# Kernel optimization log

Measured on AMD Instinct MI355X. Metric: run time of the kernel, lower is better.

The kernel has to match this reference:

```python
import jax, jax.numpy as jnp
import numpy as np

B, R, C, E, H = 2, 16, 512, 1024, 16
D = E // H  # head_dim = 64


def setup_inputs() -> dict:
    key = jax.random.key(0)
    ks = jax.random.split(key, 9)
    s = 1.0 / np.sqrt(E)
    return {
        "x": jax.random.normal(ks[0], (B, R, C, E), dtype=jnp.float32),
        "wq": jax.random.uniform(ks[1], (E, E), jnp.float32, -s, s),
        "bq": jax.random.uniform(ks[2], (E,), jnp.float32, -s, s),
        "wk": jax.random.uniform(ks[3], (E, E), jnp.float32, -s, s),
        "bk": jax.random.uniform(ks[4], (E,), jnp.float32, -s, s),
        "wv": jax.random.uniform(ks[5], (E, E), jnp.float32, -s, s),
        "bv": jax.random.uniform(ks[6], (E,), jnp.float32, -s, s),
        "wo": jax.random.uniform(ks[7], (E, E), jnp.float32, -s, s),
        "bo": jax.random.uniform(ks[8], (E,), jnp.float32, -s, s),
    }


def reference(x, wq, bq, wk, bk, wv, bv, wo, bo):
    b, r, c, e = x.shape
    # projections: [b,r,c,e] -> [b,r,h,c,d]
    def split_heads(t):
        return t.reshape(b, r, c, H, D).transpose(0, 1, 3, 2, 4)
    q = split_heads(x @ wq + bq)
    k = split_heads(x @ wk + bk)
    v = split_heads(x @ wv + bv)
    scale = 1.0 / jnp.sqrt(jnp.asarray(D, x.dtype))
    logits = jnp.einsum('brhqd,brhkd->brhqk', q, k) * scale
    probs = jax.nn.softmax(logits, axis=-1)
    ctx = jnp.einsum('brhqk,brhkd->brhqd', probs, v)
    ctx = ctx.transpose(0, 1, 3, 2, 4).reshape(b, r, c, e)
    return ctx @ wo + bo
```

## Files before the change

kernel.cpp:

```cpp
#include <hip/hip_runtime.h>
#include <hip/hip_bf16.h>
#include <hip/hip_fp16.h>
#include <math.h>

typedef _Float16 half8 __attribute__((ext_vector_type(8)));
typedef __attribute__((ext_vector_type(4))) float floatx4;

constexpr int Bc = 2, Rc = 16, Cc = 512, Ec = 1024, Hc = 16, Dc = 64;
constexpr int Mtok = Bc * Rc * Cc;
#define QSCALE 0.180336880111120425f

__device__ inline void gl_lds16(const void* g, void* l) {
  __builtin_amdgcn_global_load_lds(
      (const __attribute__((address_space(1))) void*)g,
      (__attribute__((address_space(3))) void*)l, 16, 0, 0);
}
__device__ inline unsigned short f2h(float f) {
  __half h = __float2half_rn(f);
  return *(unsigned short*)&h;
}
__device__ inline unsigned int pack_h2(float lo, float hi) {
  __half2 p = __float22half2_rn(make_float2(lo, hi));
  return *(unsigned int*)&p;
}

__global__ __launch_bounds__(256) void cvt_x(const float* __restrict__ x,
                                             unsigned short* __restrict__ xh) {
  const size_t base = ((size_t)blockIdx.x * 256 + threadIdx.x) * 8;
  float4 a = *(const float4*)(x + base);
  float4 b = *(const float4*)(x + base + 4);
  uint4 o;
  o.x = pack_h2(a.x, a.y);
  o.y = pack_h2(a.z, a.w);
  o.z = pack_h2(b.x, b.y);
  o.w = pack_h2(b.z, b.w);
  *(uint4*)(xh + base) = o;
}

__global__ __launch_bounds__(256) void wprep(
    const float* __restrict__ w0, const float* __restrict__ w1,
    const float* __restrict__ w2, const float* __restrict__ w3,
    unsigned short* __restrict__ t0, unsigned short* __restrict__ t1,
    unsigned short* __restrict__ t2, unsigned short* __restrict__ t3) {
  __shared__ float tile[64][65];
  const int z = blockIdx.z;
  const float* W = (z == 0) ? w0 : (z == 1) ? w1 : (z == 2) ? w2 : w3;
  unsigned short* T = (z == 0) ? t0 : (z == 1) ? t1 : (z == 2) ? t2 : t3;
  const int tid = threadIdx.x;
  const int bk = blockIdx.x * 64, bn = blockIdx.y * 64;
#pragma unroll
  for (int p = 0; p < 16; ++p) {
    int idx = p * 256 + tid;
    int lk = idx >> 6, ln = idx & 63;
    tile[ln][lk] = W[(size_t)(bk + lk) * 1024 + bn + ln];
  }
  __syncthreads();
#pragma unroll
  for (int p = 0; p < 16; ++p) {
    int idx = p * 256 + tid;
    int ln = idx >> 6, lk = idx & 63;
    T[(size_t)(bn + ln) * 1024 + bk + lk] = f2h(tile[ln][lk]);
  }
}

__global__ __launch_bounds__(256, 2) void gemm_qkv(
    const unsigned short* __restrict__ xh, const unsigned short* __restrict__ wqh,
    const unsigned short* __restrict__ wkh, const unsigned short* __restrict__ wvh,
    const float* __restrict__ bq, const float* __restrict__ bk,
    const float* __restrict__ bv, unsigned short* __restrict__ qout,
    unsigned short* __restrict__ kout, unsigned short* __restrict__ vout) {
  __shared__ unsigned short As[128 * 32];
  __shared__ unsigned short Bs[256 * 32];
  const int z = blockIdx.z;
  const unsigned short* Bp = (z == 0) ? wqh : (z == 1) ? wkh : wvh;
  const float* bias = (z == 0) ? bq : (z == 1) ? bk : bv;
  const int tid = threadIdx.x;
  const int wv_ = tid >> 6, ln = tid & 63;
  const int bn = blockIdx.x * 256, bm = blockIdx.y * 128;
  floatx4 acc[4][8];
#pragma unroll
  for (int i = 0; i < 4; ++i)
#pragma unroll
    for (int j = 0; j < 8; ++j) acc[i][j] = (floatx4)(0.f);

  const int wm = (wv_ >> 1) * 64, wn = (wv_ & 1) * 128;
  const int lr = ln & 15, quad = ln >> 4;
  const int fsl = ((quad ^ ((lr >> 1) & 3)) << 3);
  const int coff = (((ln & 3) ^ ((ln >> 3) & 3)) << 3);

  for (int t = 0; t < 32; ++t) {
    const int kk = t << 5;
#pragma unroll
    for (int is = 0; is < 2; ++is) {
      const int r0 = is * 64 + wv_ * 16;
      const int row = r0 + (ln >> 2);
      gl_lds16(xh + (size_t)(bm + row) * 1024 + kk + coff, As + r0 * 32);
    }
#pragma unroll
    for (int p = 0; p < 4; ++p) {
      const int r0 = p * 64 + wv_ * 16;
      const int row = r0 + (ln >> 2);
      gl_lds16(Bp + (size_t)(bn + row) * 1024 + kk + coff, Bs + r0 * 32);
    }
    __syncthreads();
    half8 af[4], bfr[8];
#pragma unroll
    for (int i = 0; i < 4; ++i)
      af[i] = *(const half8*)&As[(wm + i * 16 + lr) * 32 + fsl];
#pragma unroll
    for (int j = 0; j < 8; ++j)
      bfr[j] = *(const half8*)&Bs[(wn + j * 16 + lr) * 32 + fsl];
#pragma unroll
    for (int i = 0; i < 4; ++i)
#pragma unroll
      for (int j = 0; j < 8; ++j)
        acc[i][j] = __builtin_amdgcn_mfma_f32_16x16x32_f16(af[i], bfr[j],
                                                           acc[i][j], 0, 0, 0);
    __syncthreads();
  }

  const int q4 = quad * 4;
  const bool odd = ln & 1;
#pragma unroll
  for (int i = 0; i < 4; ++i) {
#pragma unroll
    for (int j = 0; j < 8; ++j) {
      const int col = bn + wn + j * 16 + lr;
      float v[4];
#pragma unroll
      for (int r = 0; r < 4; ++r) v[r] = acc[i][j][r] + bias[col];
      const int m0 = bm + wm + i * 16 + q4;
      const int h = col >> 6, d = col & 63;
      const int br = m0 >> 9, c0 = m0 & 511;
      const size_t hb = ((size_t)br * 16 + h) * 32768;
      if (z == 2) {
        uint2 o;
        o.x = pack_h2(v[0], v[1]);
        o.y = pack_h2(v[2], v[3]);
        *(uint2*)(vout + hb + (size_t)d * 512 + c0) = o;
      } else {
        unsigned short* outp = (z == 0) ? qout : kout;
        if (z == 0) {
#pragma unroll
          for (int r = 0; r < 4; ++r) v[r] *= QSCALE;
        }
#pragma unroll
        for (int rp = 0; rp < 2; ++rp) {
          float a = v[2 * rp], b = v[2 * rp + 1];
          float ax = __shfl_xor(a, 1), bx = __shfl_xor(b, 1);
          unsigned int u = odd ? pack_h2(bx, b) : pack_h2(a, ax);
          const int c = c0 + 2 * rp + (odd ? 1 : 0);
          const int dd = d & ~1;
          *(unsigned int*)(outp + hb + (size_t)c * 64 + dd) = u;
        }
      }
    }
  }
}

__global__ __launch_bounds__(256, 2) void gemm_out(
    const unsigned short* __restrict__ Ah, const unsigned short* __restrict__ Bh,
    const float* __restrict__ bias, float* __restrict__ Out) {
  __shared__ unsigned short As[128 * 32];
  __shared__ unsigned short Bs[256 * 32];
  const int tid = threadIdx.x;
  const int wv_ = tid >> 6, ln = tid & 63;
  const int bn = blockIdx.x * 256, bm = blockIdx.y * 128;
  floatx4 acc[4][8];
#pragma unroll
  for (int i = 0; i < 4; ++i)
#pragma unroll
    for (int j = 0; j < 8; ++j) acc[i][j] = (floatx4)(0.f);

  const int wm = (wv_ >> 1) * 64, wn = (wv_ & 1) * 128;
  const int lr = ln & 15, quad = ln >> 4;
  const int fsl = ((quad ^ ((lr >> 1) & 3)) << 3);
  const int coff = (((ln & 3) ^ ((ln >> 3) & 3)) << 3);

  for (int t = 0; t < 32; ++t) {
    const int kk = t << 5;
#pragma unroll
    for (int is = 0; is < 2; ++is) {
      const int r0 = is * 64 + wv_ * 16;
      const int row = r0 + (ln >> 2);
      gl_lds16(Ah + (size_t)(bm + row) * 1024 + kk + coff, As + r0 * 32);
    }
#pragma unroll
    for (int p = 0; p < 4; ++p) {
      const int r0 = p * 64 + wv_ * 16;
      const int row = r0 + (ln >> 2);
      gl_lds16(Bh + (size_t)(bn + row) * 1024 + kk + coff, Bs + r0 * 32);
    }
    __syncthreads();
    half8 af[4], bfr[8];
#pragma unroll
    for (int i = 0; i < 4; ++i)
      af[i] = *(const half8*)&As[(wm + i * 16 + lr) * 32 + fsl];
#pragma unroll
    for (int j = 0; j < 8; ++j)
      bfr[j] = *(const half8*)&Bs[(wn + j * 16 + lr) * 32 + fsl];
#pragma unroll
    for (int i = 0; i < 4; ++i)
#pragma unroll
      for (int j = 0; j < 8; ++j)
        acc[i][j] = __builtin_amdgcn_mfma_f32_16x16x32_f16(af[i], bfr[j],
                                                           acc[i][j], 0, 0, 0);
    __syncthreads();
  }

  const int q4 = (ln >> 4) * 4;
#pragma unroll
  for (int i = 0; i < 4; ++i)
#pragma unroll
    for (int j = 0; j < 8; ++j)
#pragma unroll
      for (int r = 0; r < 4; ++r) {
        const int m = bm + wm + i * 16 + q4 + r;
        const int col = bn + wn + j * 16 + lr;
        Out[(size_t)m * 1024 + col] = acc[i][j][r] + bias[col];
      }
}

__global__ __launch_bounds__(256, 2) void attn_mfma(
    const unsigned short* __restrict__ Qh, const unsigned short* __restrict__ Kb,
    const unsigned short* __restrict__ Vt, unsigned short* __restrict__ Ctx) {
  __shared__ unsigned short Ks[128 * 64];
  __shared__ unsigned short Vs[64 * 128];
  __shared__ unsigned short Ps[128][136];

  const int t = threadIdx.x;
  const int w = t >> 6, ln = t & 63;
  const int lane15 = ln & 15, quad = ln >> 4;
  const bool odd = ln & 1;
  const int bh = blockIdx.x >> 2;
  const int qb = (blockIdx.x & 3) * 128;

  half8 qf[2][2];
  {
    const size_t qbase =
        ((size_t)bh * 512 + qb + w * 32 + lane15) * 64 + quad * 8;
#pragma unroll
    for (int i = 0; i < 2; ++i)
#pragma unroll
      for (int c = 0; c < 2; ++c)
        qf[i][c] = *(const half8*)(Qh + qbase + (size_t)i * 16 * 64 + c * 32);
  }

  floatx4 oacc[2][4];
#pragma unroll
  for (int i = 0; i < 2; ++i)
#pragma unroll
    for (int dj = 0; dj < 4; ++dj) oacc[i][dj] = (floatx4)(0.f);
  float lsum[2][4];
#pragma unroll
  for (int i = 0; i < 2; ++i)
#pragma unroll
    for (int r = 0; r < 4; ++r) lsum[i][r] = 0.f;

  const unsigned short* kgb = Kb + (size_t)bh * 32768;
  const unsigned short* vgb = Vt + (size_t)bh * 32768;

  for (int kt = 0; kt < 512; kt += 128) {
    __syncthreads();
    {
      const unsigned short* kq = kgb + (size_t)kt * 64;
#pragma unroll
      for (int p = 0; p < 4; ++p) {
        const int s = p * 256 + t;
        const int kr = s >> 3, kc16 = s & 7;
        gl_lds16(kq + kr * 64 + ((kc16 ^ (kr & 7)) << 3), (char*)Ks + s * 16);
        const int vr = s >> 4, vc16 = s & 15;
        gl_lds16(vgb + vr * 512 + kt + ((vc16 ^ (vr & 15)) << 3),
                 (char*)Vs + s * 16);
      }
    }
    __syncthreads();

    floatx4 sacc[2][8];
#pragma unroll
    for (int i = 0; i < 2; ++i)
#pragma unroll
      for (int j = 0; j < 8; ++j) sacc[i][j] = (floatx4)(0.f);
#pragma unroll
    for (int j = 0; j < 8; ++j) {
      const int krow = j * 16 + lane15;
      const unsigned short* kr = Ks + krow * 64;
      half8 kf0 = *(const half8*)(kr + ((quad ^ (krow & 7)) << 3));
      half8 kf1 = *(const half8*)(kr + (((4 + quad) ^ (krow & 7)) << 3));
#pragma unroll
      for (int i = 0; i < 2; ++i) {
        sacc[i][j] = __builtin_amdgcn_mfma_f32_16x16x32_f16(qf[i][0], kf0,
                                                            sacc[i][j], 0, 0, 0);
        sacc[i][j] = __builtin_amdgcn_mfma_f32_16x16x32_f16(qf[i][1], kf1,
                                                            sacc[i][j], 0, 0, 0);
      }
    }

#pragma unroll
    for (int i = 0; i < 2; ++i) {
#pragma unroll
      for (int rp = 0; rp < 2; ++rp) {
        const int rA = rp * 2, rB = rA + 1;
        const int row = w * 32 + i * 16 + quad * 4 + rA + (odd ? 1 : 0);
        unsigned short* prow = &Ps[row][lane15 & ~1];
#pragma unroll
        for (int j = 0; j < 8; ++j) {
          const float pA = exp2f(sacc[i][j][rA]);
          const float pB = exp2f(sacc[i][j][rB]);
          lsum[i][rA] += pA;
          lsum[i][rB] += pB;
          const float an = __shfl_xor(pA, 1);
          const float bn = __shfl_xor(pB, 1);
          const float lo = odd ? bn : pA;
          const float hi = odd ? pB : an;
          *(unsigned int*)(prow + j * 16) = pack_h2(lo, hi);
        }
      }
    }

#pragma unroll
    for (int kc = 0; kc < 4; ++kc) {
      half8 pa0 = *(const half8*)&Ps[w * 32 + lane15][kc * 32 + quad * 8];
      half8 pa1 = *(const half8*)&Ps[w * 32 + 16 + lane15][kc * 32 + quad * 8];
#pragma unroll
      for (int dj = 0; dj < 4; ++dj) {
        const int drow = dj * 16 + lane15;
        half8 vf = *(const half8*)(
            Vs + drow * 128 + (((kc * 4 + quad) ^ (drow & 15)) << 3));
        oacc[0][dj] = __builtin_amdgcn_mfma_f32_16x16x32_f16(pa0, vf,
                                                             oacc[0][dj], 0, 0, 0);
        oacc[1][dj] = __builtin_amdgcn_mfma_f32_16x16x32_f16(pa1, vf,
                                                             oacc[1][dj], 0, 0, 0);
      }
    }
  }

  float invl[2][4];
#pragma unroll
  for (int i = 0; i < 2; ++i)
#pragma unroll
    for (int r = 0; r < 4; ++r) {
      float ls = lsum[i][r];
#pragma unroll
      for (int off = 1; off < 16; off <<= 1) ls += __shfl_xor(ls, off);
      invl[i][r] = 1.f / ls;
    }
  const int br = bh >> 4, h = bh & 15;
  const size_t mbase = (size_t)br * 512 + qb + w * 32;
#pragma unroll
  for (int i = 0; i < 2; ++i)
#pragma unroll
    for (int dj = 0; dj < 4; ++dj) {
      const int e = h * 64 + dj * 16 + lane15;
      const int ee = e & ~1;
#pragma unroll
      for (int rp = 0; rp < 2; ++rp) {
        const int rA = 2 * rp, rB = rA + 1;
        float a = oacc[i][dj][rA] * invl[i][rA];
        float b = oacc[i][dj][rB] * invl[i][rB];
        float ax = __shfl_xor(a, 1), bx = __shfl_xor(b, 1);
        unsigned int u = odd ? pack_h2(bx, b) : pack_h2(a, ax);
        const size_t m = mbase + i * 16 + quad * 4 + rA + (odd ? 1 : 0);
        *(unsigned int*)(Ctx + m * 1024 + ee) = u;
      }
    }
}

extern "C" void kernel_launch(void* const* d_in, const int* in_sizes, int n_in,
                              void* d_out, int out_size, void* d_ws,
                              size_t ws_size, hipStream_t stream) {
  const float* x = (const float*)d_in[0];
  const float* wq = (const float*)d_in[1];
  const float* bq = (const float*)d_in[2];
  const float* wk = (const float*)d_in[3];
  const float* bk = (const float*)d_in[4];
  const float* wv = (const float*)d_in[5];
  const float* bv = (const float*)d_in[6];
  const float* wo = (const float*)d_in[7];
  const float* bo = (const float*)d_in[8];
  float* out = (float*)d_out;

  char* w = (char*)d_ws;
  const size_t MiB = 1ull << 20;
  unsigned short* qbuf = (unsigned short*)(w + 0 * MiB);
  unsigned short* kbuf = (unsigned short*)(w + 32 * MiB);
  unsigned short* vtb = (unsigned short*)(w + 64 * MiB);
  unsigned short* xh = (unsigned short*)(w + 96 * MiB);
  unsigned short* ctx = (unsigned short*)(w + 128 * MiB);
  unsigned short* wqh = (unsigned short*)(w + 160 * MiB);
  unsigned short* wkh = (unsigned short*)(w + 162 * MiB);
  unsigned short* wvh = (unsigned short*)(w + 164 * MiB);
  unsigned short* woh = (unsigned short*)(w + 166 * MiB);

  cvt_x<<<8192, 256, 0, stream>>>(x, xh);
  wprep<<<dim3(16, 16, 4), 256, 0, stream>>>(wq, wk, wv, wo, wqh, wkh, wvh,
                                             woh);

  gemm_qkv<<<dim3(4, 128, 3), 256, 0, stream>>>(xh, wqh, wkh, wvh, bq, bk, bv,
                                                qbuf, kbuf, vtb);

  attn_mfma<<<2048, 256, 0, stream>>>(qbuf, kbuf, vtb, ctx);

  gemm_out<<<dim3(4, 128), 256, 0, stream>>>(ctx, woh, bo, out);
}
```

Measured before the change: 400.3 us.

## Replace QKV and output GEMMs with pipelined 256x256 double-buffered MFMA kernel

Replaces the two 128x256, single-buffered, 8-wave-free GEMMs with a templated 512-thread 256x256 tile kernel. It uses a BK=64, double-buffered LDS pipeline with interleaved global-to-LDS staging, explicit waitcnt/barrier scheduling and setprio around MFMA bursts, and a swizzled block-index mapping for L2 reuse. The QKV GEMM now treats the three weight matrices as one concatenated N=3072 operand, assuming wqh/wkh/wvh are contiguous in the workspace. The aim is to hide global load latency and raise MFMA utilisation, at the cost of 128KB LDS per block and fragile hand scheduling.

```diff
diff --git a/kernel.cpp b/kernel.cpp
--- a/kernel.cpp
+++ b/kernel.cpp
@@ -7,7 +7,6 @@
 typedef __attribute__((ext_vector_type(4))) float floatx4;
 
 constexpr int Bc = 2, Rc = 16, Cc = 512, Ec = 1024, Hc = 16, Dc = 64;
-constexpr int Mtok = Bc * Rc * Cc;
 #define QSCALE 0.180336880111120425f
 
 __device__ inline void gl_lds16(const void* g, void* l) {
@@ -63,162 +62,209 @@
   }
 }
 
-__global__ __launch_bounds__(256, 2) void gemm_qkv(
-    const unsigned short* __restrict__ xh, const unsigned short* __restrict__ wqh,
-    const unsigned short* __restrict__ wkh, const unsigned short* __restrict__ wvh,
+#define STG(OP, BUF, KT, H)                                                   \
+  {                                                                           \
+    const unsigned short* gsp_ = (OP) ? Bb : Ab;                              \
+    unsigned short* lb_ =                                                     \
+        ((OP) ? Bs : As) + (BUF) * 16384 + (H) * 8192 + w * 1024;             \
+    _Pragma("unroll") for (int l_ = 0; l_ < 2; ++l_)                          \
+        gl_lds16(gsp_ + (size_t)((H) * 128 + srow + l_ * 8) * 1024 +          \
+                     (KT) * 64 + goff,                                        \
+                 lb_ + l_ * 512);                                             \
+  }
+
+#define DSRA(BUF, MH)                                                         \
+  _Pragma("unroll") for (int i_ = 0; i_ < 4; ++i_) {                          \
+    const unsigned short* p_ =                                                \
+        As + (BUF) * 16384 + (wm + (MH) * 64 + i_ * 16 + lr) * 64;            \
+    af[i_][0] = *(const half8*)(p_ + sw0);                                    \
+    af[i_][1] = *(const half8*)(p_ + sw1);                                    \
+  }
+
+#define DSRB(BUF, NH)                                                         \
+  _Pragma("unroll") for (int j_ = 0; j_ < 2; ++j_) {                          \
+    const unsigned short* p_ =                                                \
+        Bs + (BUF) * 16384 + (wn + (NH) * 32 + j_ * 16 + lr) * 64;            \
+    bf[j_][0] = *(const half8*)(p_ + sw0);                                    \
+    bf[j_][1] = *(const half8*)(p_ + sw1);                                    \
+  }
+
+#define MFMA16(MH, NH)                                                        \
+  _Pragma("unroll") for (int i_ = 0; i_ < 4; ++i_)                            \
+      _Pragma("unroll") for (int j_ = 0; j_ < 2; ++j_) {                      \
+    acc[(MH)*4 + i_][(NH)*2 + j_] = __builtin_amdgcn_mfma_f32_16x16x32_f16(   \
+        af[i_][0], bf[j_][0], acc[(MH)*4 + i_][(NH)*2 + j_], 0, 0, 0);        \
+    acc[(MH)*4 + i_][(NH)*2 + j_] = __builtin_amdgcn_mfma_f32_16x16x32_f16(   \
+        af[i_][1], bf[j_][1], acc[(MH)*4 + i_][(NH)*2 + j_], 0, 0, 0);        \
+  }
+
+#define WAIT_LGKM0                                                            \
+  {                                                                           \
+    asm volatile("s_waitcnt lgkmcnt(0)" ::: "memory");                        \
+    __builtin_amdgcn_sched_barrier(0);                                        \
+  }
+#define WAIT_VM(N)                                                            \
+  {                                                                           \
+    asm volatile("s_waitcnt vmcnt(" #N ")" ::: "memory");                     \
+    __builtin_amdgcn_sched_barrier(0);                                        \
+  }
+
+#define TILE(T, BUF, S12, S4, VM0)                                            \
+  {                                                                           \
+                                                                      \
+    DSRA(BUF, 0);                                                             \
+    DSRB(BUF, 0);                                                             \
+    if (S12) {                                                                \
+      STG(0, (BUF) ^ 1, (T) + 1, 1);                                          \
+      STG(1, (BUF) ^ 1, (T) + 1, 0);                                          \
+    }                                                                         \
+    __builtin_amdgcn_s_barrier();                                             \
+    WAIT_LGKM0;                                                               \
+    __builtin_amdgcn_s_setprio(1);                                            \
+    MFMA16(0, 0);                                                             \
+    __builtin_amdgcn_s_setprio(0);                                            \
+    __builtin_amdgcn_s_barrier();                                             \
+    __builtin_amdgcn_sched_barrier(0);                                        \
+                                                                      \
+    DSRB(BUF, 1);                                                             \
+    if (S12) { STG(1, (BUF) ^ 1, (T) + 1, 1); }                               \
+    __builtin_amdgcn_s_barrier();                                             \
+    WAIT_LGKM0;                                                               \
+    __builtin_amdgcn_s_setprio(1);                                            \
+    MFMA16(0, 1);                                                             \
+    __builtin_amdgcn_s_setprio(0);                                            \
+    __builtin_amdgcn_s_barrier();                                             \
+    __builtin_amdgcn_sched_barrier(0);                                        \
+                                                                      \
+    DSRA(BUF, 1);                                                             \
+    __builtin_amdgcn_s_barrier();                                             \
+    WAIT_LGKM0;                                                               \
+    __builtin_amdgcn_s_setprio(1);                                            \
+    MFMA16(1, 1);                                                             \
+    __builtin_amdgcn_s_setprio(0);                                            \
+    __builtin_amdgcn_s_barrier();                                             \
+    __builtin_amdgcn_sched_barrier(0);                                        \
+                                                                      \
+    DSRB(BUF, 0);                                                             \
+    if (S4) { STG(0, BUF, (T) + 2, 0); }                                      \
+    if (VM0) { WAIT_VM(0); } else { WAIT_VM(2); }                             \
+    __builtin_amdgcn_s_barrier();                                             \
+    WAIT_LGKM0;                                                               \
+    __builtin_amdgcn_s_setprio(1);                                            \
+    MFMA16(1, 0);                                                             \
+    __builtin_amdgcn_s_setprio(0);                                            \
+    __builtin_amdgcn_s_barrier();                                             \
+    __builtin_amdgcn_sched_barrier(0);                                        \
+  }
+
+template <int MODE>
+__global__ __launch_bounds__(512, 2) void gemm256(
+    const unsigned short* __restrict__ gA, const unsigned short* __restrict__ gB,
     const float* __restrict__ bq, const float* __restrict__ bk,
     const float* __restrict__ bv, unsigned short* __restrict__ qout,
-    unsigned short* __restrict__ kout, unsigned short* __restrict__ vout) {
-  __shared__ unsigned short As[128 * 32];
-  __shared__ unsigned short Bs[256 * 32];
-  const int z = blockIdx.z;
-  const unsigned short* Bp = (z == 0) ? wqh : (z == 1) ? wkh : wvh;
-  const float* bias = (z == 0) ? bq : (z == 1) ? bk : bv;
+    unsigned short* __restrict__ kout, unsigned short* __restrict__ vout,
+    float* __restrict__ fout, const float* __restrict__ bo) {
+  __shared__ unsigned short As[2 * 16384];
+  __shared__ unsigned short Bs[2 * 16384];
   const int tid = threadIdx.x;
-  const int wv_ = tid >> 6, ln = tid & 63;
-  const int bn = blockIdx.x * 256, bm = blockIdx.y * 128;
-  floatx4 acc[4][8];
-#pragma unroll
-  for (int i = 0; i < 4; ++i)
-#pragma unroll
-    for (int j = 0; j < 8; ++j) acc[i][j] = (floatx4)(0.f);
-
-  const int wm = (wv_ >> 1) * 64, wn = (wv_ & 1) * 128;
+  const int w = tid >> 6, ln = tid & 63;
   const int lr = ln & 15, quad = ln >> 4;
-  const int fsl = ((quad ^ ((lr >> 1) & 3)) << 3);
-  const int coff = (((ln & 3) ^ ((ln >> 3) & 3)) << 3);
-
-  for (int t = 0; t < 32; ++t) {
-    const int kk = t << 5;
-#pragma unroll
-    for (int is = 0; is < 2; ++is) {
-      const int r0 = is * 64 + wv_ * 16;
-      const int row = r0 + (ln >> 2);
-      gl_lds16(xh + (size_t)(bm + row) * 1024 + kk + coff, As + r0 * 32);
-    }
-#pragma unroll
-    for (int p = 0; p < 4; ++p) {
-      const int r0 = p * 64 + wv_ * 16;
-      const int row = r0 + (ln >> 2);
-      gl_lds16(Bp + (size_t)(bn + row) * 1024 + kk + coff, Bs + r0 * 32);
-    }
-    __syncthreads();
-    half8 af[4], bfr[8];
-#pragma unroll
-    for (int i = 0; i < 4; ++i)
-      af[i] = *(const half8*)&As[(wm + i * 16 + lr) * 32 + fsl];
-#pragma unroll
-    for (int j = 0; j < 8; ++j)
-      bfr[j] = *(const half8*)&Bs[(wn + j * 16 + lr) * 32 + fsl];
-#pragma unroll
-    for (int i = 0; i < 4; ++i)
-#pragma unroll
-      for (int j = 0; j < 8; ++j)
-        acc[i][j] = __builtin_amdgcn_mfma_f32_16x16x32_f16(af[i], bfr[j],
-                                                           acc[i][j], 0, 0, 0);
-    __syncthreads();
-  }
+  const int wm = (w >> 2) * 128, wn = (w & 3) * 64;
+  int bm, bn;
+  if (MODE == 0) {
+    const int swz = (blockIdx.x & 7) * 96 + (blockIdx.x >> 3);
+    bm = (swz / 12) * 256;
+    bn = (swz % 12) * 256;
+  } else {
+    const int swz = (blockIdx.x & 7) * 32 + (blockIdx.x >> 3);
+    bm = (swz >> 2) * 256;
+    bn = (swz & 3) * 256;
+  }
+  const unsigned short* Ab = gA + (size_t)bm * 1024;
+  const unsigned short* Bb = gB + (size_t)bn * 1024;
+  const int goff = (ln >> 3) * 1024 + (((ln & 7) ^ (ln >> 3)) << 3);
+  const int srow = w * 16;
+  const int sw0 = ((quad ^ (lr & 7)) << 3);
+  const int sw1 = (((4 | quad) ^ (lr & 7)) << 3);
+
+  floatx4 acc[8][4];
+#pragma unroll
+  for (int i = 0; i < 8; ++i)
+#pragma unroll
+    for (int j = 0; j < 4; ++j) acc[i][j] = (floatx4)(0.f);
+  half8 af[4][2], bf[2][2];
+
+  STG(0, 0, 0, 0);
+  STG(0, 0, 0, 1);
+  STG(1, 0, 0, 0);
+  STG(1, 0, 0, 1);
+  STG(0, 1, 1, 0);
+  WAIT_VM(2);
+  __builtin_amdgcn_s_barrier();
+  __builtin_amdgcn_sched_barrier(0);
+
+  for (int t = 0; t < 7; ++t) {
+    const int T0 = 2 * t;
+    TILE(T0, 0, 1, 1, 0);
+    TILE(T0 + 1, 1, 1, 1, 0);
+  }
+  TILE(14, 0, 1, 0, 1);
+  TILE(15, 1, 0, 0, 1);
 
   const int q4 = quad * 4;
   const bool odd = ln & 1;
-#pragma unroll
-  for (int i = 0; i < 4; ++i) {
-#pragma unroll
-    for (int j = 0; j < 8; ++j) {
-      const int col = bn + wn + j * 16 + lr;
-      float v[4];
-#pragma unroll
-      for (int r = 0; r < 4; ++r) v[r] = acc[i][j][r] + bias[col];
-      const int m0 = bm + wm + i * 16 + q4;
-      const int h = col >> 6, d = col & 63;
-      const int br = m0 >> 9, c0 = m0 & 511;
-      const size_t hb = ((size_t)br * 16 + h) * 32768;
-      if (z == 2) {
-        uint2 o;
-        o.x = pack_h2(v[0], v[1]);
-        o.y = pack_h2(v[2], v[3]);
-        *(uint2*)(vout + hb + (size_t)d * 512 + c0) = o;
-      } else {
-        unsigned short* outp = (z == 0) ? qout : kout;
-        if (z == 0) {
-#pragma unroll
-          for (int r = 0; r < 4; ++r) v[r] *= QSCALE;
+  if constexpr (MODE == 0) {
+    const int z = bn >> 10;
+    const float* bias = (z == 0) ? bq : (z == 1) ? bk : bv;
+    const int czb = (bn & 1023) + wn;
+#pragma unroll
+    for (int i = 0; i < 8; ++i) {
+#pragma unroll
+      for (int j = 0; j < 4; ++j) {
+        const int colz = czb + j * 16 + lr;
+        float v[4];
+#pragma unroll
+        for (int r = 0; r < 4; ++r) v[r] = acc[i][j][r] + bias[colz];
+        const int m0 = bm + wm + i * 16 + q4;
+        const int h = colz >> 6, d = colz & 63;
+        const int brr = m0 >> 9, c0 = m0 & 511;
+        const size_t hb = ((size_t)brr * 16 + h) * 32768;
+        if (z == 2) {
+          uint2 o;
+          o.x = pack_h2(v[0], v[1]);
+          o.y = pack_h2(v[2], v[3]);
+          *(uint2*)(vout + hb + (size_t)d * 512 + c0) = o;
+        } else {
+          unsigned short* outp = (z == 0) ? qout : kout;
+          if (z == 0) {
+#pragma unroll
+            for (int r = 0; r < 4; ++r) v[r] *= QSCALE;
+          }
+#pragma unroll
+          for (int rp = 0; rp < 2; ++rp) {
+            float a = v[2 * rp], b = v[2 * rp + 1];
+            float ax = __shfl_xor(a, 1), bx = __shfl_xor(b, 1);
+            unsigned int u = odd ? pack_h2(bx, b) : pack_h2(a, ax);
+            const int c = c0 + 2 * rp + (odd ? 1 : 0);
+            const int dd = d & ~1;
+            *(unsigned int*)(outp + hb + (size_t)c * 64 + dd) = u;
+          }
         }
-#pragma unroll
-        for (int rp = 0; rp < 2; ++rp) {
-          float a = v[2 * rp], b = v[2 * rp + 1];
-          float ax = __shfl_xor(a, 1), bx = __shfl_xor(b, 1);
-          unsigned int u = odd ? pack_h2(bx, b) : pack_h2(a, ax);
-          const int c = c0 + 2 * rp + (odd ? 1 : 0);
-          const int dd = d & ~1;
-          *(unsigned int*)(outp + hb + (size_t)c * 64 + dd) = u;
+      }
+    }
+  } else {
+#pragma unroll
+    for (int i = 0; i < 8; ++i)
+#pragma unroll
+      for (int j = 0; j < 4; ++j) {
+        const int col = bn + wn + j * 16 + lr;
+#pragma unroll
+        for (int r = 0; r < 4; ++r) {
+          const int m = bm + wm + i * 16 + q4 + r;
+          fout[(size_t)m * 1024 + col] = acc[i][j][r] + bo[col];
         }
       }
-    }
-  }
-}
-
-__global__ __launch_bounds__(256, 2) void gemm_out(
-    const unsigned short* __restrict__ Ah, const unsigned short* __restrict__ Bh,
-    const float* __restrict__ bias, float* __restrict__ Out) {
-  __shared__ unsigned short As[128 * 32];
-  __shared__ unsigned short Bs[256 * 32];
-  const int tid = threadIdx.x;
-  const int wv_ = tid >> 6, ln = tid & 63;
-  const int bn = blockIdx.x * 256, bm = blockIdx.y * 128;
-  floatx4 acc[4][8];
-#pragma unroll
-  for (int i = 0; i < 4; ++i)
-#pragma unroll
-    for (int j = 0; j < 8; ++j) acc[i][j] = (floatx4)(0.f);
-
-  const int wm = (wv_ >> 1) * 64, wn = (wv_ & 1) * 128;
-  const int lr = ln & 15, quad = ln >> 4;
-  const int fsl = ((quad ^ ((lr >> 1) & 3)) << 3);
-  const int coff = (((ln & 3) ^ ((ln >> 3) & 3)) << 3);
-
-  for (int t = 0; t < 32; ++t) {
-    const int kk = t << 5;
-#pragma unroll
-    for (int is = 0; is < 2; ++is) {
-      const int r0 = is * 64 + wv_ * 16;
-      const int row = r0 + (ln >> 2);
-      gl_lds16(Ah + (size_t)(bm + row) * 1024 + kk + coff, As + r0 * 32);
-    }
-#pragma unroll
-    for (int p = 0; p < 4; ++p) {
-      const int r0 = p * 64 + wv_ * 16;
-      const int row = r0 + (ln >> 2);
-      gl_lds16(Bh + (size_t)(bn + row) * 1024 + kk + coff, Bs + r0 * 32);
-    }
-    __syncthreads();
-    half8 af[4], bfr[8];
-#pragma unroll
-    for (int i = 0; i < 4; ++i)
-      af[i] = *(const half8*)&As[(wm + i * 16 + lr) * 32 + fsl];
-#pragma unroll
-    for (int j = 0; j < 8; ++j)
-      bfr[j] = *(const half8*)&Bs[(wn + j * 16 + lr) * 32 + fsl];
-#pragma unroll
-    for (int i = 0; i < 4; ++i)
-#pragma unroll
-      for (int j = 0; j < 8; ++j)
-        acc[i][j] = __builtin_amdgcn_mfma_f32_16x16x32_f16(af[i], bfr[j],
-                                                           acc[i][j], 0, 0, 0);
-    __syncthreads();
-  }
-
-  const int q4 = (ln >> 4) * 4;
-#pragma unroll
-  for (int i = 0; i < 4; ++i)
-#pragma unroll
-    for (int j = 0; j < 8; ++j)
-#pragma unroll
-      for (int r = 0; r < 4; ++r) {
-        const int m = bm + wm + i * 16 + q4 + r;
-        const int col = bn + wn + j * 16 + lr;
-        Out[(size_t)m * 1024 + col] = acc[i][j][r] + bias[col];
-      }
+  }
 }
 
 __global__ __launch_bounds__(256, 2) void attn_mfma(
@@ -396,10 +442,11 @@
   wprep<<<dim3(16, 16, 4), 256, 0, stream>>>(wq, wk, wv, wo, wqh, wkh, wvh,
                                              woh);
 
-  gemm_qkv<<<dim3(4, 128, 3), 256, 0, stream>>>(xh, wqh, wkh, wvh, bq, bk, bv,
-                                                qbuf, kbuf, vtb);
+  gemm256<0><<<768, 512, 0, stream>>>(xh, wqh, bq, bk, bv, qbuf, kbuf, vtb,
+                                      nullptr, nullptr);
 
   attn_mfma<<<2048, 256, 0, stream>>>(qbuf, kbuf, vtb, ctx);
 
-  gemm_out<<<dim3(4, 128), 256, 0, stream>>>(ctx, woh, bo, out);
-}
+  gemm256<1><<<256, 512, 0, stream>>>(ctx, woh, nullptr, nullptr, nullptr,
+                                      nullptr, nullptr, nullptr, out, bo);
+}
```

Result: no change. 398.4 us (-0.5%).
